# Kernel tuning notes

Hardware: AMD Instinct MI355X
Metric: run time of the kernel (lower is better)

Reference implementation:

```python
import jax, jax.numpy as jnp
import numpy as np

B, S, D_MODEL, H = 2, 2048, 1024, 16
HD = D_MODEL // H  # 64


def rotate_half(x):
    # pairs (x_even, x_odd) -> (-x_odd, x_even), interleaved back
    x1 = x[..., ::2]
    x2 = x[..., 1::2]
    return jnp.stack([-x2, x1], axis=-1).reshape(x.shape)


def rope_sin_cos(seq_len, head_dim):
    pos = jnp.arange(seq_len, dtype=jnp.float32)
    dim = jnp.arange(head_dim, dtype=jnp.float32)
    theta = 10000.0 ** (-2.0 * jnp.floor(dim / 2.0) / head_dim)
    angles = pos[:, None] * theta[None, :]  # [S, HD]
    return jnp.sin(angles), jnp.cos(angles)


def setup_inputs():
    key = jax.random.key(0)
    ks = jax.random.split(key, 6)
    w_scale = 1.0 / np.sqrt(D_MODEL)
    x = jax.random.normal(ks[0], (B, S, D_MODEL), jnp.float32)
    # causal mask: 1.0 where attention is disallowed (j > i)
    mask = (1.0 - jnp.tril(jnp.ones((S, S), jnp.float32)))[None, None, :, :]
    wq = jax.random.normal(ks[1], (D_MODEL, D_MODEL), jnp.float32) * w_scale
    wk = jax.random.normal(ks[2], (D_MODEL, D_MODEL), jnp.float32) * w_scale
    wv = jax.random.normal(ks[3], (D_MODEL, D_MODEL), jnp.float32) * w_scale
    wo = jax.random.normal(ks[4], (D_MODEL, D_MODEL), jnp.float32) * w_scale
    zeros = jnp.zeros((D_MODEL,), jnp.float32)
    return dict(x=x, mask=mask, wq=wq, bq=zeros, wk=wk, bk=zeros,
                wv=wv, bv=zeros, wo=wo, bo=zeros)


def reference(x, mask, wq, bq, wk, bk, wv, bv, wo, bo):
    b, s, _ = x.shape

    def split_heads(t):  # [B,S,D] -> [B,H,S,HD]
        return t.reshape(b, s, H, HD).transpose(0, 2, 1, 3)

    q = split_heads(x @ wq + bq)
    k = split_heads(x @ wk + bk)
    v = split_heads(x @ wv + bv)

    sin, cos = rope_sin_cos(s, HD)
    sin = sin[None, None, :, :]
    cos = cos[None, None, :, :]
    q = q * cos + rotate_half(q) * sin
    k = k * cos + rotate_half(k) * sin

    logits = jnp.einsum('bhqd,bhkd->bhqk', q, k) / jnp.sqrt(jnp.float32(HD))
    logits = logits + mask * (-1e9)
    attn = jax.nn.softmax(logits, axis=-1)
    out = jnp.einsum('bhqk,bhkd->bhqd', attn, v)  # [B,H,S,HD]
    out = out.transpose(0, 2, 1, 3).reshape(b, s, D_MODEL)
    return out @ wo + bo
```

## Files before the change

### kernel.cpp

```cpp
#include <hip/hip_runtime.h>
#include <hip/hip_bf16.h>


#define S_ 2048
#define DM 1024
#define HD 64

typedef __attribute__((ext_vector_type(8))) short short8;
typedef __attribute__((ext_vector_type(4))) float floatx4;

__device__ __forceinline__ unsigned short f2b(float x) {
  union { __hip_bfloat16 h; unsigned short u; } cv;
  cv.h = __float2bfloat16(x);
  return cv.u;
}

__device__ __forceinline__ void gload_lds16(const unsigned short* g, unsigned short* l) {
  typedef const __attribute__((address_space(1))) unsigned int* gp_t;
  typedef __attribute__((address_space(3))) unsigned int* lp_t;
  __builtin_amdgcn_global_load_lds((gp_t)(const void*)g, (lp_t)(void*)l, 16, 0, 0);
}

__global__ void prep_kernel(const float* __restrict__ x,
                            const float* __restrict__ w0, const float* __restrict__ w1,
                            const float* __restrict__ w2, const float* __restrict__ w3,
                            unsigned short* __restrict__ xc,
                            unsigned short* __restrict__ wt,
                            float2* __restrict__ rope) {
  const int bid = blockIdx.x;
  if (bid < 4096) {
    int i = (bid * 256 + threadIdx.x) * 4;
    float4 v = *(const float4*)(x + i);
    ushort4 o;
    o.x = f2b(v.x); o.y = f2b(v.y); o.z = f2b(v.z); o.w = f2b(v.w);
    *(ushort4*)(xc + i) = o;
  } else if (bid < 8192) {
    __shared__ float tile[32][33];
    const int rem = bid - 4096;
    const int z = rem >> 10;
    const int bx = (rem & 1023) & 31;
    const int by = (rem & 1023) >> 5;
    const float* W = (z == 0) ? w0 : (z == 1) ? w1 : (z == 2) ? w2 : w3;
    unsigned short* Wt = wt + (size_t)z * DM * DM;
    const int tx = threadIdx.x & 31;
    const int ty = threadIdx.x >> 5;
    const int k0 = bx * 32;
    const int c0 = by * 32;
#pragma unroll
    for (int i = 0; i < 4; ++i)
      tile[ty + i * 8][tx] = W[(size_t)(k0 + ty + i * 8) * DM + c0 + tx];
    __syncthreads();
#pragma unroll
    for (int i = 0; i < 4; ++i)
      Wt[(size_t)(c0 + ty + i * 8) * DM + k0 + tx] = f2b(tile[tx][ty + i * 8]);
  } else {
    int i = (bid - 8192) * 256 + threadIdx.x;
    int s = i >> 5, d2 = i & 31;
    float th = expf(-(float)d2 * (9.210340371976184f / 32.0f));
    float sn, cs;
    sincosf((float)s * th, &sn, &cs);
    rope[i] = make_float2(cs, sn);
  }
}

__global__ __launch_bounds__(256, 3) void gemm_qkv(
    const unsigned short* __restrict__ A, const unsigned short* __restrict__ Wt,
    const float* __restrict__ bq, const float* __restrict__ bk,
    const float* __restrict__ bv, const float2* __restrict__ rope,
    unsigned short* __restrict__ QKV) {
  __shared__ __attribute__((aligned(16))) unsigned short As[128 * 64];
  __shared__ __attribute__((aligned(16))) unsigned short Bs[128 * 64];
  const int r0 = blockIdx.x * 128;
  const int c0 = blockIdx.y * 128;
  const int t = threadIdx.x;
  const int lane = t & 63;
  const int wv = t >> 6;
  const int wr = (wv >> 1) * 64;
  const int wc = (wv & 1) * 64;
  const int lr = lane & 15;
  const int lg = lane >> 4;

  const int srow = wv * 32 + (lane >> 3);
  const int sseg = ((lane & 7) ^ (lane >> 3)) * 8;
  const unsigned short* Ag = A + (size_t)(r0 + srow) * DM + sseg;
  const unsigned short* Bg = Wt + (size_t)(c0 + srow) * DM + sseg;
  unsigned short* lA = &As[wv * 32 * 64];
  unsigned short* lB = &Bs[wv * 32 * 64];

  floatx4 acc[4][4] = {};
  const int fswz = (lr & 7) << 4;

  for (int k0 = 0; k0 < DM; k0 += 64) {
#pragma unroll
    for (int j = 0; j < 4; ++j) {
      gload_lds16(Ag + k0 + j * 8 * DM, lA + j * 8 * 64);
      gload_lds16(Bg + k0 + j * 8 * DM, lB + j * 8 * 64);
    }
    __syncthreads();
#pragma unroll
    for (int kk = 0; kk < 2; ++kk) {
      short8 af[4], bf[4];
#pragma unroll
      for (int m = 0; m < 4; ++m)
        af[m] = *(const short8*)((char*)As + (wr + m * 16 + lr) * 128 +
                                 ((kk * 64 + lg * 16) ^ fswz));
#pragma unroll
      for (int n = 0; n < 4; ++n)
        bf[n] = *(const short8*)((char*)Bs + (wc + n * 16 + lr) * 128 +
                                 ((kk * 64 + lg * 16) ^ fswz));
#pragma unroll
      for (int m = 0; m < 4; ++m)
#pragma unroll
        for (int n = 0; n < 4; ++n)
          acc[m][n] = __builtin_amdgcn_mfma_f32_16x16x32_bf16(af[m], bf[n], acc[m][n], 0, 0, 0);
    }
    __syncthreads();
  }

  const int mat = blockIdx.y >> 3;
  const float* bias = (mat == 0) ? bq : (mat == 1) ? bk : bv;
  const int rbase = r0 + wr + lg * 4;
  const int cbase = c0 + wc + lr;
#pragma unroll
  for (int n = 0; n < 4; ++n) {
    const int c = cbase + n * 16;
    const int cc = c & (DM - 1);
    const float bvv = bias[cc];
    const int d = c & 63;
    const int h = cc >> 6;
#pragma unroll
    for (int m = 0; m < 4; ++m) {
#pragma unroll
      for (int i = 0; i < 4; ++i) {
        const int r = rbase + m * 16 + i;
        const int s = r & (S_ - 1);
        const int b = r >> 11;
        float v = acc[m][n][i] + bvv;
        float pv = __shfl_xor(v, 1);
        if (mat < 2) {
          float2 cssn = rope[s * 32 + (d >> 1)];
          v = (d & 1) ? fmaf(v, cssn.x, pv * cssn.y) : fmaf(v, cssn.x, -pv * cssn.y);
          if (mat == 0) v *= 0.18033688011112042f;
        }
        QKV[((size_t)((mat << 5) | (b << 4) | h) * S_ + s) * HD + d] = f2b(v);
      }
    }
  }
}

__global__ __launch_bounds__(256, 3) void gemm_out(
    const unsigned short* __restrict__ A, const unsigned short* __restrict__ Wt,
    const float* __restrict__ bias, float* __restrict__ out) {
  __shared__ __attribute__((aligned(16))) unsigned short As[128 * 64];
  __shared__ __attribute__((aligned(16))) unsigned short Bs[128 * 64];
  const int r0 = blockIdx.x * 128;
  const int c0 = blockIdx.y * 128;
  const int t = threadIdx.x;
  const int lane = t & 63;
  const int wv = t >> 6;
  const int wr = (wv >> 1) * 64;
  const int wc = (wv & 1) * 64;
  const int lr = lane & 15;
  const int lg = lane >> 4;

  const int srow = wv * 32 + (lane >> 3);
  const int sseg = ((lane & 7) ^ (lane >> 3)) * 8;
  const unsigned short* Ag = A + (size_t)(r0 + srow) * DM + sseg;
  const unsigned short* Bg = Wt + (size_t)(c0 + srow) * DM + sseg;
  unsigned short* lA = &As[wv * 32 * 64];
  unsigned short* lB = &Bs[wv * 32 * 64];

  floatx4 acc[4][4] = {};
  const int fswz = (lr & 7) << 4;

  for (int k0 = 0; k0 < DM; k0 += 64) {
#pragma unroll
    for (int j = 0; j < 4; ++j) {
      gload_lds16(Ag + k0 + j * 8 * DM, lA + j * 8 * 64);
      gload_lds16(Bg + k0 + j * 8 * DM, lB + j * 8 * 64);
    }
    __syncthreads();
#pragma unroll
    for (int kk = 0; kk < 2; ++kk) {
      short8 af[4], bf[4];
#pragma unroll
      for (int m = 0; m < 4; ++m)
        af[m] = *(const short8*)((char*)As + (wr + m * 16 + lr) * 128 +
                                 ((kk * 64 + lg * 16) ^ fswz));
#pragma unroll
      for (int n = 0; n < 4; ++n)
        bf[n] = *(const short8*)((char*)Bs + (wc + n * 16 + lr) * 128 +
                                 ((kk * 64 + lg * 16) ^ fswz));
#pragma unroll
      for (int m = 0; m < 4; ++m)
#pragma unroll
        for (int n = 0; n < 4; ++n)
          acc[m][n] = __builtin_amdgcn_mfma_f32_16x16x32_bf16(af[m], bf[n], acc[m][n], 0, 0, 0);
    }
    __syncthreads();
  }

  const int rbase = r0 + wr + lg * 4;
  const int cbase = c0 + wc + lr;
#pragma unroll
  for (int n = 0; n < 4; ++n) {
    const int c = cbase + n * 16;
    const float bvv = bias[c];
#pragma unroll
    for (int m = 0; m < 4; ++m) {
#pragma unroll
      for (int i = 0; i < 4; ++i) {
        const int r = rbase + m * 16 + i;
        out[(size_t)r * DM + c] = acc[m][n][i] + bvv;
      }
    }
  }
}

#define ATTN_STEP(TT, BUF, KLA, KLB)                                           \
  do {                                                                         \
    {                  \
      char* Vb = (char*)Vs[BUF];                                               \
      const unsigned* ua = (const unsigned*)&va;                               \
      const unsigned* ub = (const unsigned*)&vb;                               \
      _Pragma("unroll") for (int j = 0; j < 8; ++j) {                          \
        unsigned pk = __builtin_amdgcn_perm(                                   \
            ub[j >> 1], ua[j >> 1], (j & 1) ? 0x07060302u : 0x05040100u);      \
        *(unsigned*)(Vb + (oct * 8 + j) * 128 + ((4 * kp) ^ (j << 4))) = pk;   \
      }                                                                        \
    }                                                                          \
    if ((TT) < qt) {                                \
      va = *(const short8*)(Vpref);                                            \
      vb = *(const short8*)(Vpref + 64);                                       \
      Vpref += 4096;                                                           \
    }                                                                          \
                        \
    asm volatile("s_waitcnt lgkmcnt(0)" ::: "memory");                         \
    __builtin_amdgcn_s_barrier();                                              \
                 \
    if ((TT) < qt) asm volatile("s_waitcnt vmcnt(2)" ::: "memory");            \
    else           asm volatile("s_waitcnt vmcnt(0)" ::: "memory");            \
    __builtin_amdgcn_sched_barrier(0);                                         \
    if ((TT) < qt) {                   \
      gload_lds16(Kpref, KLA);                                                 \
      gload_lds16(Kpref + 2048, KLB);                                          \
      Kpref += 4096;                                                           \
    }                                                                          \
                     \
    floatx4 s[4] = {};                                                         \
    __builtin_amdgcn_s_setprio(1);                                             \
    _Pragma("unroll") for (int kk = 0; kk < 2; ++kk) {                         \
      _Pragma("unroll") for (int n = 0; n < 4; ++n) {                          \
        int r = n * 16 + lr;                                                   \
        short8 kf = *(const short8*)((char*)Ks[BUF] + r * 128 +                \
                                     ((kk * 64 + lg * 16) ^ ((r & 7) << 4)));  \
        s[n] = __builtin_amdgcn_mfma_f32_16x16x32_bf16(kf, qf[kk], s[n], 0, 0, 0); \
      }                                                                        \
    }                                                                          \
    __builtin_amdgcn_s_setprio(0);                                             \
    if ((TT) == qt) {                                                          \
      _Pragma("unroll") for (int n = 0; n < 4; ++n)                            \
        _Pragma("unroll") for (int i = 0; i < 4; ++i)                          \
          if (n * 16 + lg * 4 + i > qin) s[n][i] = -1e30f;                     \
    }                                                                          \
                                \
    float ta = fmaxf(fmaxf(s[0][0], s[0][1]), s[0][2]);                        \
    float tb = fmaxf(fmaxf(s[0][3], s[1][0]), s[1][1]);                        \
    float tc = fmaxf(fmaxf(s[1][2], s[1][3]), s[2][0]);                        \
    float td = fmaxf(fmaxf(s[2][1], s[2][2]), s[2][3]);                        \
    float te = fmaxf(fmaxf(s[3][0], s[3][1]), s[3][2]);                        \
    float tm = fmaxf(fmaxf(ta, tb), tc);                                       \
    tm = fmaxf(fmaxf(tm, td), te);                                             \
    tm = fmaxf(tm, s[3][3]);                                                   \
    tm = fmaxf(tm, __shfl_xor(tm, 16));                                        \
    tm = fmaxf(tm, __shfl_xor(tm, 32));                                        \
    if (__any(tm > m + 8.f)) {                          \
      const float mn = fmaxf(m, tm);                                           \
      const float al = exp2f(m - mn);                                          \
      m = mn;                                                                  \
      lsum *= al;                                                              \
      _Pragma("unroll") for (int dd = 0; dd < 4; ++dd) o[dd] *= al;            \
    }                                                                          \
    float ps = 0.f;                                                            \
    _Pragma("unroll") for (int n = 0; n < 4; ++n) {                            \
      _Pragma("unroll") for (int i = 0; i < 4; ++i) {                          \
        float p = exp2f(s[n][i] - m);                                          \
        s[n][i] = p;                                                           \
        ps += p;                                                               \
      }                                                                        \
    }                                                                          \
    lsum += ps;                                                                \
                    \
    _Pragma("unroll") for (int n = 0; n < 4; ++n) {                            \
      _Pragma("unroll") for (int hh = 0; hh < 2; ++hh) {                       \
        unsigned pk = (unsigned)f2b(s[n][2 * hh]) |                            \
                      ((unsigned)f2b(s[n][2 * hh + 1]) << 16);                 \
        *(unsigned*)(Pw + lr * 128 +                                           \
                     (((n * 16 + lg * 4 + 2 * hh) * 2) ^ pswz)) = pk;          \
      }                                                                        \
    }                                                                          \
    short8 pb[2];                                                              \
    _Pragma("unroll") for (int kk = 0; kk < 2; ++kk)                           \
      pb[kk] = *(const short8*)(Pw + lr * 128 + ((kk * 64 + lg * 16) ^ pswz)); \
    __builtin_amdgcn_s_setprio(1);                                             \
    _Pragma("unroll") for (int kk = 0; kk < 2; ++kk)                           \
      _Pragma("unroll") for (int dd = 0; dd < 4; ++dd) {                       \
        int d = dd * 16 + lr;                                                  \
        short8 vbf = *(const short8*)((char*)Vs[BUF] + d * 128 +               \
                                      ((kk * 64 + lg * 16) ^ ((d & 7) << 4))); \
        o[dd] = __builtin_amdgcn_mfma_f32_16x16x32_bf16(vbf, pb[kk], o[dd], 0, 0, 0); \
      }                                                                        \
    __builtin_amdgcn_s_setprio(0);                                             \
  } while (0)

__global__ __launch_bounds__(256, 4) void attn_kernel(
    const unsigned short* __restrict__ Q, const unsigned short* __restrict__ K,
    const unsigned short* __restrict__ V, unsigned short* __restrict__ AttnC) {
  __shared__ __attribute__((aligned(16))) unsigned short Ks[2][64 * 64];
  __shared__ __attribute__((aligned(16))) unsigned short Vs[2][64 * 64];
  __shared__ __attribute__((aligned(16))) unsigned short Ps[4][16 * 64];

  const int bh = blockIdx.x;
  const int qt = 31 - (int)blockIdx.y;
  const int tid = threadIdx.x;
  const int w = tid >> 6;
  const int l = tid & 63;
  const int lg = l >> 4;
  const int lr = l & 15;
  const size_t base = (size_t)bh * S_ * HD;
  const int qin = w * 16 + lr;

  short8 qf[2];
  {
    const unsigned short* Qrow =
        Q + base + (size_t)(qt * 64 + w * 16 + lr) * HD + lg * 8;
    qf[0] = *(const short8*)(Qrow);
    qf[1] = *(const short8*)(Qrow + 32);
  }

  floatx4 o[4] = {};
  float m = -1e30f, lsum = 0.f;

  const int krow = tid >> 3;
  const int kseg = tid & 7;
  const unsigned short* Kpref = K + base + krow * 64 + ((kseg ^ (krow & 7)) * 8);
  unsigned short* const kld0a = &Ks[0][w * 512];
  unsigned short* const kld0b = &Ks[0][2048 + w * 512];
  unsigned short* const kld1a = &Ks[1][w * 512];
  unsigned short* const kld1b = &Ks[1][2048 + w * 512];

  const int oct = tid >> 5;
  const int kp = tid & 31;
  const unsigned short* Vpref = V + base + 2 * kp * 64 + oct * 8;

  short8 va = *(const short8*)(Vpref);
  short8 vb = *(const short8*)(Vpref + 64);
  Vpref += 4096;
  gload_lds16(Kpref, kld0a);
  gload_lds16(Kpref + 2048, kld0b);
  Kpref += 4096;

  char* const Pw = (char*)Ps[w];
  const int pswz = (lr & 7) << 4;

  int t = 0;
#pragma unroll 1
  for (; t + 1 <= qt; t += 2) {
    ATTN_STEP(t, 0, kld1a, kld1b);
    ATTN_STEP(t + 1, 1, kld0a, kld0b);
  }
  if (t <= qt) ATTN_STEP(t, 0, kld1a, kld1b);

  lsum += __shfl_xor(lsum, 16);
  lsum += __shfl_xor(lsum, 32);
  const float inv = 1.f / lsum;
  unsigned short* orow =
      AttnC + (size_t)((bh >> 4) * S_ + qt * 64 + w * 16 + lr) * DM + (bh & 15) * HD;
#pragma unroll
  for (int dd = 0; dd < 4; ++dd) {
    unsigned int w0 = (unsigned int)f2b(o[dd][0] * inv) |
                      ((unsigned int)f2b(o[dd][1] * inv) << 16);
    unsigned int w1 = (unsigned int)f2b(o[dd][2] * inv) |
                      ((unsigned int)f2b(o[dd][3] * inv) << 16);
    *(uint2*)(orow + dd * 16 + lg * 4) = make_uint2(w0, w1);
  }
}

extern "C" void kernel_launch(void* const* d_in, const int* in_sizes, int n_in,
                              void* d_out, int out_size, void* d_ws, size_t ws_size,
                              hipStream_t stream) {
  const float* x = (const float*)d_in[0];
  const float* wq = (const float*)d_in[2];
  const float* bq = (const float*)d_in[3];
  const float* wk = (const float*)d_in[4];
  const float* bk = (const float*)d_in[5];
  const float* wv = (const float*)d_in[6];
  const float* bv = (const float*)d_in[7];
  const float* wo = (const float*)d_in[8];
  const float* bo = (const float*)d_in[9];

  char* ws = (char*)d_ws;
  const size_t MB = 1024ull * 1024ull;
  unsigned short* Xc = (unsigned short*)(ws);
  unsigned short* Wt = (unsigned short*)(ws + 8 * MB);
  unsigned short* QKVb = (unsigned short*)(ws + 16 * MB);
  unsigned short* Ac = (unsigned short*)(ws + 40 * MB);
  float2* rope = (float2*)(ws + 48 * MB);

  prep_kernel<<<8448, 256, 0, stream>>>(x, wq, wk, wv, wo, Xc, Wt, rope);
  gemm_qkv<<<dim3(32, 24), 256, 0, stream>>>(Xc, Wt, bq, bk, bv, rope, QKVb);
  attn_kernel<<<dim3(32, 32), 256, 0, stream>>>(
      QKVb, QKVb + 32ull * S_ * HD, QKVb + 64ull * S_ * HD, Ac);
  gemm_out<<<dim3(32, 8), 256, 0, stream>>>(Ac, Wt + 3ull * DM * DM, bo, (float*)d_out);
}
```

Before: 114.3 us.

## Pair causal query tiles per block and switch attention to 32x32 MFMA

Each attention block now handles two query tiles, ya and 31-ya, with two waves per tile, so every block streams the same K/V range and the causal workload is balanced across the halved grid. QK and PV use 32x32x16 bf16 MFMAs, and the P operand is rearranged in registers with cross-lane shuffles instead of going through a per-wave LDS buffer. The diagonal tile skips the upper masked half for one sub-wave. Launch bounds drop to 2 blocks per CU, which raises register use and may reduce occupancy. Waves working on the shorter tile sit idle while the block continues loading tiles for the longer one.

New measurement: 126.5 us. 10.7% more time.

```diff
diff --git a/kernel.cpp b/kernel.cpp
--- a/kernel.cpp
+++ b/kernel.cpp
@@ -8,6 +8,7 @@
 
 typedef __attribute__((ext_vector_type(8))) short short8;
 typedef __attribute__((ext_vector_type(4))) float floatx4;
+typedef __attribute__((ext_vector_type(16))) float floatx16;
 
 __device__ __forceinline__ unsigned short f2b(float x) {
   union { __hip_bfloat16 h; unsigned short u; } cv;
@@ -217,6 +218,27 @@
   }
 }
 
+#define PVK(KSEG, PKS)                                                         \
+  do {                                                                         \
+    const int c4 = ((KSEG) & 1) * 4;                                           \
+    unsigned xv0 = hi ? (PKS)[c4 + 0] : (PKS)[c4 + 2];                         \
+    unsigned xv1 = hi ? (PKS)[c4 + 1] : (PKS)[c4 + 3];                         \
+    unsigned rv0 = (unsigned)__shfl_xor((int)xv0, 32);                         \
+    unsigned rv1 = (unsigned)__shfl_xor((int)xv1, 32);                         \
+    short8 bp;                                                                 \
+    unsigned* bpd = (unsigned*)&bp;                                            \
+    bpd[0] = hi ? rv0 : (PKS)[c4 + 0];                                         \
+    bpd[1] = hi ? rv1 : (PKS)[c4 + 1];                                         \
+    bpd[2] = hi ? (PKS)[c4 + 2] : rv0;                                         \
+    bpd[3] = hi ? (PKS)[c4 + 3] : rv1;                                         \
+    short8 vf0 = *(const short8*)(Vbb + q32 * 128 +                            \
+                                  (((KSEG)*32 + hi * 16) ^ kswz));             \
+    short8 vf1 = *(const short8*)(Vbb + (32 + q32) * 128 +                     \
+                                  (((KSEG)*32 + hi * 16) ^ kswz));             \
+    o0 = __builtin_amdgcn_mfma_f32_32x32x16_bf16(vf0, bp, o0, 0, 0, 0);        \
+    o1 = __builtin_amdgcn_mfma_f32_32x32x16_bf16(vf1, bp, o1, 0, 0, 0);        \
+  } while (0)
+
 #define ATTN_STEP(TT, BUF, KLA, KLB)                                           \
   do {                                                                         \
     {                  \
@@ -224,134 +246,150 @@
       const unsigned* ua = (const unsigned*)&va;                               \
       const unsigned* ub = (const unsigned*)&vb;                               \
       _Pragma("unroll") for (int j = 0; j < 8; ++j) {                          \
-        unsigned pk = __builtin_amdgcn_perm(                                   \
+        unsigned pkv = __builtin_amdgcn_perm(                                  \
             ub[j >> 1], ua[j >> 1], (j & 1) ? 0x07060302u : 0x05040100u);      \
-        *(unsigned*)(Vb + (oct * 8 + j) * 128 + ((4 * kp) ^ (j << 4))) = pk;   \
+        *(unsigned*)(Vb + (oct * 8 + j) * 128 + ((4 * kp) ^ (j << 4))) = pkv;  \
       }                                                                        \
     }                                                                          \
-    if ((TT) < qt) {                                \
+    if ((TT) < NTm1) {                              \
       va = *(const short8*)(Vpref);                                            \
       vb = *(const short8*)(Vpref + 64);                                       \
       Vpref += 4096;                                                           \
     }                                                                          \
-                        \
     asm volatile("s_waitcnt lgkmcnt(0)" ::: "memory");                         \
     __builtin_amdgcn_s_barrier();                                              \
-                 \
-    if ((TT) < qt) asm volatile("s_waitcnt vmcnt(2)" ::: "memory");            \
-    else           asm volatile("s_waitcnt vmcnt(0)" ::: "memory");            \
+    if ((TT) < NTm1) asm volatile("s_waitcnt vmcnt(2)" ::: "memory");          \
+    else             asm volatile("s_waitcnt vmcnt(0)" ::: "memory");          \
     __builtin_amdgcn_sched_barrier(0);                                         \
-    if ((TT) < qt) {                   \
+    if ((TT) < NTm1) {                 \
       gload_lds16(Kpref, KLA);                                                 \
       gload_lds16(Kpref + 2048, KLB);                                          \
       Kpref += 4096;                                                           \
     }                                                                          \
-                     \
-    floatx4 s[4] = {};                                                         \
-    __builtin_amdgcn_s_setprio(1);                                             \
-    _Pragma("unroll") for (int kk = 0; kk < 2; ++kk) {                         \
-      _Pragma("unroll") for (int n = 0; n < 4; ++n) {                          \
-        int r = n * 16 + lr;                                                   \
-        short8 kf = *(const short8*)((char*)Ks[BUF] + r * 128 +                \
-                                     ((kk * 64 + lg * 16) ^ ((r & 7) << 4)));  \
-        s[n] = __builtin_amdgcn_mfma_f32_16x16x32_bf16(kf, qf[kk], s[n], 0, 0, 0); \
-      }                                                                        \
+    if ((TT) <= myqs) {                                                        \
+      const bool diag = ((TT) == myqs);                                        \
+      const bool halfq = diag && (sub == 0);                                   \
+      const char* Kb = (const char*)Ks[BUF];                                   \
+      floatx16 s0 = {}, s1 = {};                                               \
+      __builtin_amdgcn_s_setprio(1);                                           \
+      _Pragma("unroll") for (int ds = 0; ds < 4; ++ds) {                       \
+        short8 kf = *(const short8*)(Kb + q32 * 128 +                          \
+                                     ((ds * 32 + hi * 16) ^ kswz));            \
+        s0 = __builtin_amdgcn_mfma_f32_32x32x16_bf16(kf, qf[ds], s0, 0, 0, 0); \
+      }                                                                        \
+      if (!halfq) {                                                            \
+        _Pragma("unroll") for (int ds = 0; ds < 4; ++ds) {                     \
+          short8 kf = *(const short8*)(Kb + (32 + q32) * 128 +                 \
+                                       ((ds * 32 + hi * 16) ^ kswz));          \
+          s1 = __builtin_amdgcn_mfma_f32_32x32x16_bf16(kf, qf[ds], s1, 0, 0, 0); \
+        }                                                                      \
+      }                                                                        \
+      __builtin_amdgcn_s_setprio(0);                                           \
+      if (diag) {        \
+        if (sub == 0) {                                                        \
+          _Pragma("unroll") for (int r = 0; r < 16; ++r) {                     \
+            int key32 = (r & 3) + 8 * (r >> 2) + 4 * hi;                       \
+            if (key32 > q32) s0[r] = -1e30f;                                   \
+          }                                                                    \
+        } else {                                                               \
+          _Pragma("unroll") for (int r = 0; r < 16; ++r) {                     \
+            int key32 = (r & 3) + 8 * (r >> 2) + 4 * hi;                       \
+            if (key32 > q32) s1[r] = -1e30f;                                   \
+          }                                                                    \
+        }                                                                      \
+      }                                                                        \
+              \
+      float tm = s0[0];                                                        \
+      _Pragma("unroll") for (int r = 1; r < 16; ++r) tm = fmaxf(tm, s0[r]);    \
+      if (!halfq) {                                                            \
+        _Pragma("unroll") for (int r = 0; r < 16; ++r) tm = fmaxf(tm, s1[r]);  \
+      }                                                                        \
+      tm = fmaxf(tm, __shfl_xor(tm, 32));                                      \
+      if (__any(tm > m + 8.f)) {                                               \
+        const float mn = fmaxf(m, tm);                                         \
+        const float al = exp2f(m - mn);                                        \
+        m = mn;                                                                \
+        lsum *= al;                                                            \
+        _Pragma("unroll") for (int r = 0; r < 16; ++r) {                       \
+          o0[r] *= al;                                                         \
+          o1[r] *= al;                                                         \
+        }                                                                      \
+      }                                                                        \
+      float ps = 0.f;                                                          \
+      _Pragma("unroll") for (int r = 0; r < 16; ++r) {                         \
+        float p = exp2f(s0[r] - m);                                            \
+        s0[r] = p;                                                             \
+        ps += p;                                                               \
+      }                                                                        \
+      if (!halfq) {                                                            \
+        _Pragma("unroll") for (int r = 0; r < 16; ++r) {                       \
+          float p = exp2f(s1[r] - m);                                          \
+          s1[r] = p;                                                           \
+          ps += p;                                                             \
+        }                                                                      \
+      }                                                                        \
+      lsum += ps;                                                              \
+                  \
+      unsigned pk0[8], pk1[8];                                                 \
+      _Pragma("unroll") for (int p = 0; p < 8; ++p)                            \
+        pk0[p] = (unsigned)f2b(s0[2 * p]) | ((unsigned)f2b(s0[2 * p + 1]) << 16); \
+      if (!halfq) {                                                            \
+        _Pragma("unroll") for (int p = 0; p < 8; ++p)                          \
+          pk1[p] = (unsigned)f2b(s1[2 * p]) | ((unsigned)f2b(s1[2 * p + 1]) << 16); \
+      }                                                                        \
+      const char* Vbb = (const char*)Vs[BUF];                                  \
+      __builtin_amdgcn_s_setprio(1);                                           \
+      PVK(0, pk0);                                                             \
+      PVK(1, pk0);                                                             \
+      if (!halfq) {                                                            \
+        PVK(2, pk1);                                                           \
+        PVK(3, pk1);                                                           \
+      }                                                                        \
+      __builtin_amdgcn_s_setprio(0);                                           \
     }                                                                          \
-    __builtin_amdgcn_s_setprio(0);                                             \
-    if ((TT) == qt) {                                                          \
-      _Pragma("unroll") for (int n = 0; n < 4; ++n)                            \
-        _Pragma("unroll") for (int i = 0; i < 4; ++i)                          \
-          if (n * 16 + lg * 4 + i > qin) s[n][i] = -1e30f;                     \
-    }                                                                          \
-                                \
-    float ta = fmaxf(fmaxf(s[0][0], s[0][1]), s[0][2]);                        \
-    float tb = fmaxf(fmaxf(s[0][3], s[1][0]), s[1][1]);                        \
-    float tc = fmaxf(fmaxf(s[1][2], s[1][3]), s[2][0]);                        \
-    float td = fmaxf(fmaxf(s[2][1], s[2][2]), s[2][3]);                        \
-    float te = fmaxf(fmaxf(s[3][0], s[3][1]), s[3][2]);                        \
-    float tm = fmaxf(fmaxf(ta, tb), tc);                                       \
-    tm = fmaxf(fmaxf(tm, td), te);                                             \
-    tm = fmaxf(tm, s[3][3]);                                                   \
-    tm = fmaxf(tm, __shfl_xor(tm, 16));                                        \
-    tm = fmaxf(tm, __shfl_xor(tm, 32));                                        \
-    if (__any(tm > m + 8.f)) {                          \
-      const float mn = fmaxf(m, tm);                                           \
-      const float al = exp2f(m - mn);                                          \
-      m = mn;                                                                  \
-      lsum *= al;                                                              \
-      _Pragma("unroll") for (int dd = 0; dd < 4; ++dd) o[dd] *= al;            \
-    }                                                                          \
-    float ps = 0.f;                                                            \
-    _Pragma("unroll") for (int n = 0; n < 4; ++n) {                            \
-      _Pragma("unroll") for (int i = 0; i < 4; ++i) {                          \
-        float p = exp2f(s[n][i] - m);                                          \
-        s[n][i] = p;                                                           \
-        ps += p;                                                               \
-      }                                                                        \
-    }                                                                          \
-    lsum += ps;                                                                \
-                    \
-    _Pragma("unroll") for (int n = 0; n < 4; ++n) {                            \
-      _Pragma("unroll") for (int hh = 0; hh < 2; ++hh) {                       \
-        unsigned pk = (unsigned)f2b(s[n][2 * hh]) |                            \
-                      ((unsigned)f2b(s[n][2 * hh + 1]) << 16);                 \
-        *(unsigned*)(Pw + lr * 128 +                                           \
-                     (((n * 16 + lg * 4 + 2 * hh) * 2) ^ pswz)) = pk;          \
-      }                                                                        \
-    }                                                                          \
-    short8 pb[2];                                                              \
-    _Pragma("unroll") for (int kk = 0; kk < 2; ++kk)                           \
-      pb[kk] = *(const short8*)(Pw + lr * 128 + ((kk * 64 + lg * 16) ^ pswz)); \
-    __builtin_amdgcn_s_setprio(1);                                             \
-    _Pragma("unroll") for (int kk = 0; kk < 2; ++kk)                           \
-      _Pragma("unroll") for (int dd = 0; dd < 4; ++dd) {                       \
-        int d = dd * 16 + lr;                                                  \
-        short8 vbf = *(const short8*)((char*)Vs[BUF] + d * 128 +               \
-                                      ((kk * 64 + lg * 16) ^ ((d & 7) << 4))); \
-        o[dd] = __builtin_amdgcn_mfma_f32_16x16x32_bf16(vbf, pb[kk], o[dd], 0, 0, 0); \
-      }                                                                        \
-    __builtin_amdgcn_s_setprio(0);                                             \
   } while (0)
 
-__global__ __launch_bounds__(256, 4) void attn_kernel(
+__global__ __launch_bounds__(256, 2) void attn_kernel(
     const unsigned short* __restrict__ Q, const unsigned short* __restrict__ K,
     const unsigned short* __restrict__ V, unsigned short* __restrict__ AttnC) {
   __shared__ __attribute__((aligned(16))) unsigned short Ks[2][64 * 64];
   __shared__ __attribute__((aligned(16))) unsigned short Vs[2][64 * 64];
-  __shared__ __attribute__((aligned(16))) unsigned short Ps[4][16 * 64];
 
   const int bh = blockIdx.x;
-  const int qt = 31 - (int)blockIdx.y;
+  const int ya = (int)blockIdx.y;
+  const int yb = 31 - ya;
   const int tid = threadIdx.x;
   const int w = tid >> 6;
-  const int l = tid & 63;
-  const int lg = l >> 4;
-  const int lr = l & 15;
+  const int lane = tid & 63;
+  const int hi = lane >> 5;
+  const int q32 = lane & 31;
+  const int kswz = (lane & 7) << 4;
+  const int sub = w & 1;
+  const int myqs = (w < 2) ? ya : yb;
+  const int NTm1 = yb;
   const size_t base = (size_t)bh * S_ * HD;
-  const int qin = w * 16 + lr;
-
-  short8 qf[2];
+
+  short8 qf[4];
   {
     const unsigned short* Qrow =
-        Q + base + (size_t)(qt * 64 + w * 16 + lr) * HD + lg * 8;
-    qf[0] = *(const short8*)(Qrow);
-    qf[1] = *(const short8*)(Qrow + 32);
-  }
-
-  floatx4 o[4] = {};
+        Q + base + (size_t)(myqs * 64 + sub * 32 + q32) * HD + hi * 8;
+#pragma unroll
+    for (int ds = 0; ds < 4; ++ds) qf[ds] = *(const short8*)(Qrow + ds * 16);
+  }
+
+  floatx16 o0 = {}, o1 = {};
   float m = -1e30f, lsum = 0.f;
 
   const int krow = tid >> 3;
-  const int kseg = tid & 7;
-  const unsigned short* Kpref = K + base + krow * 64 + ((kseg ^ (krow & 7)) * 8);
+  const int kseg8 = tid & 7;
+  const int oct = tid >> 5;
+  const int kp = tid & 31;
+  const unsigned short* Kpref = K + base + krow * 64 + ((kseg8 ^ (krow & 7)) * 8);
+  const unsigned short* Vpref = V + base + 2 * kp * 64 + oct * 8;
   unsigned short* const kld0a = &Ks[0][w * 512];
   unsigned short* const kld0b = &Ks[0][2048 + w * 512];
   unsigned short* const kld1a = &Ks[1][w * 512];
   unsigned short* const kld1b = &Ks[1][2048 + w * 512];
-
-  const int oct = tid >> 5;
-  const int kp = tid & 31;
-  const unsigned short* Vpref = V + base + 2 * kp * 64 + oct * 8;
 
   short8 va = *(const short8*)(Vpref);
   short8 vb = *(const short8*)(Vpref + 64);
@@ -360,29 +398,37 @@
   gload_lds16(Kpref + 2048, kld0b);
   Kpref += 4096;
 
-  char* const Pw = (char*)Ps[w];
-  const int pswz = (lr & 7) << 4;
-
   int t = 0;
 #pragma unroll 1
-  for (; t + 1 <= qt; t += 2) {
+  for (; t + 1 <= NTm1; t += 2) {
     ATTN_STEP(t, 0, kld1a, kld1b);
     ATTN_STEP(t + 1, 1, kld0a, kld0b);
   }
-  if (t <= qt) ATTN_STEP(t, 0, kld1a, kld1b);
-
-  lsum += __shfl_xor(lsum, 16);
+  if (t <= NTm1) ATTN_STEP(t, 0, kld1a, kld1b);
+
   lsum += __shfl_xor(lsum, 32);
   const float inv = 1.f / lsum;
+  const int qglob = myqs * 64 + sub * 32 + q32;
   unsigned short* orow =
-      AttnC + (size_t)((bh >> 4) * S_ + qt * 64 + w * 16 + lr) * DM + (bh & 15) * HD;
-#pragma unroll
-  for (int dd = 0; dd < 4; ++dd) {
-    unsigned int w0 = (unsigned int)f2b(o[dd][0] * inv) |
-                      ((unsigned int)f2b(o[dd][1] * inv) << 16);
-    unsigned int w1 = (unsigned int)f2b(o[dd][2] * inv) |
-                      ((unsigned int)f2b(o[dd][3] * inv) << 16);
-    *(uint2*)(orow + dd * 16 + lg * 4) = make_uint2(w0, w1);
+      AttnC + (size_t)((bh >> 4) * S_ + qglob) * DM + (bh & 15) * HD;
+#pragma unroll
+  for (int g = 0; g < 4; ++g) {
+    {
+      const int d0 = 8 * g + 4 * hi;
+      unsigned w0 = (unsigned)f2b(o0[4 * g + 0] * inv) |
+                    ((unsigned)f2b(o0[4 * g + 1] * inv) << 16);
+      unsigned w1 = (unsigned)f2b(o0[4 * g + 2] * inv) |
+                    ((unsigned)f2b(o0[4 * g + 3] * inv) << 16);
+      *(uint2*)(orow + d0) = make_uint2(w0, w1);
+    }
+    {
+      const int d0 = 32 + 8 * g + 4 * hi;
+      unsigned w0 = (unsigned)f2b(o1[4 * g + 0] * inv) |
+                    ((unsigned)f2b(o1[4 * g + 1] * inv) << 16);
+      unsigned w1 = (unsigned)f2b(o1[4 * g + 2] * inv) |
+                    ((unsigned)f2b(o1[4 * g + 3] * inv) << 16);
+      *(uint2*)(orow + d0) = make_uint2(w0, w1);
+    }
   }
 }
 
@@ -409,7 +455,7 @@
 
   prep_kernel<<<8448, 256, 0, stream>>>(x, wq, wk, wv, wo, Xc, Wt, rope);
   gemm_qkv<<<dim3(32, 24), 256, 0, stream>>>(Xc, Wt, bq, bk, bv, rope, QKVb);
-  attn_kernel<<<dim3(32, 32), 256, 0, stream>>>(
+  attn_kernel<<<dim3(32, 16), 256, 0, stream>>>(
       QKVb, QKVb + 32ull * S_ * HD, QKVb + 64ull * S_ * HD, Ac);
   gemm_out<<<dim3(32, 8), 256, 0, stream>>>(Ac, Wt + 3ull * DM * DM, bo, (float*)d_out);
 }
```

## Enlarge attention query tile to 128 rows with two row-groups per wave

Applied to the files above, without the earlier changes.

The attention kernel now processes 128 query rows per block instead of 64, with each wave handling two 16-row groups that share every K/V fragment loaded from LDS. This halves the K/V global and LDS traffic per query row and doubles the MFMA work per fragment load. Waves whose diagonal tile comes earlier skip compute on later key tiles. In exchange, register pressure roughly doubles (launch bounds drop from 4 to 2 blocks per CU), there are half as many blocks, and causal load imbalance inside a block grows.

After: 130.4 us. 14.1% more time.

```diff
diff --git a/kernel.cpp b/kernel.cpp
--- a/kernel.cpp
+++ b/kernel.cpp
@@ -224,134 +224,154 @@
       const unsigned* ua = (const unsigned*)&va;                               \
       const unsigned* ub = (const unsigned*)&vb;                               \
       _Pragma("unroll") for (int j = 0; j < 8; ++j) {                          \
-        unsigned pk = __builtin_amdgcn_perm(                                   \
+        unsigned pkv = __builtin_amdgcn_perm(                                  \
             ub[j >> 1], ua[j >> 1], (j & 1) ? 0x07060302u : 0x05040100u);      \
-        *(unsigned*)(Vb + (oct * 8 + j) * 128 + ((4 * kp) ^ (j << 4))) = pk;   \
+        *(unsigned*)(Vb + (oct * 8 + j) * 128 + ((4 * kp) ^ (j << 4))) = pkv;  \
       }                                                                        \
     }                                                                          \
-    if ((TT) < qt) {                                \
+    if ((TT) < NTm1) {                              \
       va = *(const short8*)(Vpref);                                            \
       vb = *(const short8*)(Vpref + 64);                                       \
       Vpref += 4096;                                                           \
     }                                                                          \
-                        \
     asm volatile("s_waitcnt lgkmcnt(0)" ::: "memory");                         \
     __builtin_amdgcn_s_barrier();                                              \
-                 \
-    if ((TT) < qt) asm volatile("s_waitcnt vmcnt(2)" ::: "memory");            \
-    else           asm volatile("s_waitcnt vmcnt(0)" ::: "memory");            \
+    if ((TT) < NTm1) asm volatile("s_waitcnt vmcnt(2)" ::: "memory");          \
+    else             asm volatile("s_waitcnt vmcnt(0)" ::: "memory");          \
     __builtin_amdgcn_sched_barrier(0);                                         \
-    if ((TT) < qt) {                   \
+    if ((TT) < NTm1) {                 \
       gload_lds16(Kpref, KLA);                                                 \
       gload_lds16(Kpref + 2048, KLB);                                          \
       Kpref += 4096;                                                           \
     }                                                                          \
-                     \
-    floatx4 s[4] = {};                                                         \
-    __builtin_amdgcn_s_setprio(1);                                             \
-    _Pragma("unroll") for (int kk = 0; kk < 2; ++kk) {                         \
+    if ((TT) <= dtw) {                                                         \
+                            \
+      floatx4 slo[4] = {}, shi[4] = {};                                        \
+      __builtin_amdgcn_s_setprio(1);                                           \
+      _Pragma("unroll") for (int kk = 0; kk < 2; ++kk) {                       \
+        _Pragma("unroll") for (int n = 0; n < 4; ++n) {                        \
+          int r = n * 16 + lr;                                                 \
+          short8 kf = *(const short8*)((char*)Ks[BUF] + r * 128 +              \
+                                       ((kk * 64 + lg * 16) ^ ((r & 7) << 4)));\
+          slo[n] = __builtin_amdgcn_mfma_f32_16x16x32_bf16(kf, qflo[kk], slo[n], 0, 0, 0); \
+          shi[n] = __builtin_amdgcn_mfma_f32_16x16x32_bf16(kf, qfhi[kk], shi[n], 0, 0, 0); \
+        }                                                                      \
+      }                                                                        \
+      __builtin_amdgcn_s_setprio(0);                                           \
+      if ((TT) == dtw) {                                      \
+        _Pragma("unroll") for (int n = 0; n < 4; ++n)                          \
+          _Pragma("unroll") for (int i = 0; i < 4; ++i) {                      \
+            int ki = n * 16 + lg * 4 + i;                                      \
+            if (ki > qinlo) slo[n][i] = -1e30f;                                \
+            if (ki > qinlo + 16) shi[n][i] = -1e30f;                           \
+          }                                                                    \
+      }                                                                        \
+                                       \
+      float tlo = fmaxf(fmaxf(slo[0][0], slo[0][1]), fmaxf(slo[0][2], slo[0][3])); \
+      float thi = fmaxf(fmaxf(shi[0][0], shi[0][1]), fmaxf(shi[0][2], shi[0][3])); \
+      _Pragma("unroll") for (int n = 1; n < 4; ++n) {                          \
+        tlo = fmaxf(tlo, fmaxf(fmaxf(slo[n][0], slo[n][1]),                    \
+                               fmaxf(slo[n][2], slo[n][3])));                  \
+        thi = fmaxf(thi, fmaxf(fmaxf(shi[n][0], shi[n][1]),                    \
+                               fmaxf(shi[n][2], shi[n][3])));                  \
+      }                                                                        \
+      tlo = fmaxf(tlo, __shfl_xor(tlo, 16));                                   \
+      tlo = fmaxf(tlo, __shfl_xor(tlo, 32));                                   \
+      thi = fmaxf(thi, __shfl_xor(thi, 16));                                   \
+      thi = fmaxf(thi, __shfl_xor(thi, 32));                                   \
+      if (__any((tlo > mlo + 8.f) || (thi > mhi + 8.f))) {                     \
+        const float nlo = fmaxf(mlo, tlo), nhi = fmaxf(mhi, thi);              \
+        const float alo = exp2f(mlo - nlo), ahi = exp2f(mhi - nhi);            \
+        mlo = nlo; mhi = nhi;                                                  \
+        llo *= alo; lhi *= ahi;                                                \
+        _Pragma("unroll") for (int dd = 0; dd < 4; ++dd) {                     \
+          olo[dd] *= alo;                                                      \
+          ohi[dd] *= ahi;                                                      \
+        }                                                                      \
+      }                                                                        \
+      float pslo = 0.f, pshi = 0.f;                                            \
       _Pragma("unroll") for (int n = 0; n < 4; ++n) {                          \
-        int r = n * 16 + lr;                                                   \
-        short8 kf = *(const short8*)((char*)Ks[BUF] + r * 128 +                \
-                                     ((kk * 64 + lg * 16) ^ ((r & 7) << 4)));  \
-        s[n] = __builtin_amdgcn_mfma_f32_16x16x32_bf16(kf, qf[kk], s[n], 0, 0, 0); \
-      }                                                                        \
+        _Pragma("unroll") for (int i = 0; i < 4; ++i) {                        \
+          float plo = exp2f(slo[n][i] - mlo);                                  \
+          float phi = exp2f(shi[n][i] - mhi);                                  \
+          slo[n][i] = plo; shi[n][i] = phi;                                    \
+          pslo += plo; pshi += phi;                                            \
+        }                                                                      \
+      }                                                                        \
+      llo += pslo; lhi += pshi;                                                \
+       \
+      _Pragma("unroll") for (int n = 0; n < 4; ++n) {                          \
+        _Pragma("unroll") for (int hh = 0; hh < 2; ++hh) {                     \
+          int cb = ((n * 16 + lg * 4 + 2 * hh) * 2) ^ pswz;                    \
+          unsigned plo = (unsigned)f2b(slo[n][2 * hh]) |                       \
+                         ((unsigned)f2b(slo[n][2 * hh + 1]) << 16);            \
+          unsigned phi = (unsigned)f2b(shi[n][2 * hh]) |                       \
+                         ((unsigned)f2b(shi[n][2 * hh + 1]) << 16);            \
+          *(unsigned*)(Pw + lr * 128 + cb) = plo;                              \
+          *(unsigned*)(Pw + (lr + 16) * 128 + cb) = phi;                       \
+        }                                                                      \
+      }                                                                        \
+      short8 pblo[2], pbhi[2];                                                 \
+      _Pragma("unroll") for (int kk = 0; kk < 2; ++kk) {                       \
+        pblo[kk] = *(const short8*)(Pw + lr * 128 + ((kk * 64 + lg * 16) ^ pswz)); \
+        pbhi[kk] = *(const short8*)(Pw + (lr + 16) * 128 + ((kk * 64 + lg * 16) ^ pswz)); \
+      }                                                                        \
+                             \
+      __builtin_amdgcn_s_setprio(1);                                           \
+      _Pragma("unroll") for (int kk = 0; kk < 2; ++kk)                         \
+        _Pragma("unroll") for (int dd = 0; dd < 4; ++dd) {                     \
+          int d = dd * 16 + lr;                                                \
+          short8 vbf = *(const short8*)((char*)Vs[BUF] + d * 128 +             \
+                                        ((kk * 64 + lg * 16) ^ ((d & 7) << 4))); \
+          olo[dd] = __builtin_amdgcn_mfma_f32_16x16x32_bf16(vbf, pblo[kk], olo[dd], 0, 0, 0); \
+          ohi[dd] = __builtin_amdgcn_mfma_f32_16x16x32_bf16(vbf, pbhi[kk], ohi[dd], 0, 0, 0); \
+        }                                                                      \
+      __builtin_amdgcn_s_setprio(0);                                           \
     }                                                                          \
-    __builtin_amdgcn_s_setprio(0);                                             \
-    if ((TT) == qt) {                                                          \
-      _Pragma("unroll") for (int n = 0; n < 4; ++n)                            \
-        _Pragma("unroll") for (int i = 0; i < 4; ++i)                          \
-          if (n * 16 + lg * 4 + i > qin) s[n][i] = -1e30f;                     \
-    }                                                                          \
-                                \
-    float ta = fmaxf(fmaxf(s[0][0], s[0][1]), s[0][2]);                        \
-    float tb = fmaxf(fmaxf(s[0][3], s[1][0]), s[1][1]);                        \
-    float tc = fmaxf(fmaxf(s[1][2], s[1][3]), s[2][0]);                        \
-    float td = fmaxf(fmaxf(s[2][1], s[2][2]), s[2][3]);                        \
-    float te = fmaxf(fmaxf(s[3][0], s[3][1]), s[3][2]);                        \
-    float tm = fmaxf(fmaxf(ta, tb), tc);                                       \
-    tm = fmaxf(fmaxf(tm, td), te);                                             \
-    tm = fmaxf(tm, s[3][3]);                                                   \
-    tm = fmaxf(tm, __shfl_xor(tm, 16));                                        \
-    tm = fmaxf(tm, __shfl_xor(tm, 32));                                        \
-    if (__any(tm > m + 8.f)) {                          \
-      const float mn = fmaxf(m, tm);                                           \
-      const float al = exp2f(m - mn);                                          \
-      m = mn;                                                                  \
-      lsum *= al;                                                              \
-      _Pragma("unroll") for (int dd = 0; dd < 4; ++dd) o[dd] *= al;            \
-    }                                                                          \
-    float ps = 0.f;                                                            \
-    _Pragma("unroll") for (int n = 0; n < 4; ++n) {                            \
-      _Pragma("unroll") for (int i = 0; i < 4; ++i) {                          \
-        float p = exp2f(s[n][i] - m);                                          \
-        s[n][i] = p;                                                           \
-        ps += p;                                                               \
-      }                                                                        \
-    }                                                                          \
-    lsum += ps;                                                                \
-                    \
-    _Pragma("unroll") for (int n = 0; n < 4; ++n) {                            \
-      _Pragma("unroll") for (int hh = 0; hh < 2; ++hh) {                       \
-        unsigned pk = (unsigned)f2b(s[n][2 * hh]) |                            \
-                      ((unsigned)f2b(s[n][2 * hh + 1]) << 16);                 \
-        *(unsigned*)(Pw + lr * 128 +                                           \
-                     (((n * 16 + lg * 4 + 2 * hh) * 2) ^ pswz)) = pk;          \
-      }                                                                        \
-    }                                                                          \
-    short8 pb[2];                                                              \
-    _Pragma("unroll") for (int kk = 0; kk < 2; ++kk)                           \
-      pb[kk] = *(const short8*)(Pw + lr * 128 + ((kk * 64 + lg * 16) ^ pswz)); \
-    __builtin_amdgcn_s_setprio(1);                                             \
-    _Pragma("unroll") for (int kk = 0; kk < 2; ++kk)                           \
-      _Pragma("unroll") for (int dd = 0; dd < 4; ++dd) {                       \
-        int d = dd * 16 + lr;                                                  \
-        short8 vbf = *(const short8*)((char*)Vs[BUF] + d * 128 +               \
-                                      ((kk * 64 + lg * 16) ^ ((d & 7) << 4))); \
-        o[dd] = __builtin_amdgcn_mfma_f32_16x16x32_bf16(vbf, pb[kk], o[dd], 0, 0, 0); \
-      }                                                                        \
-    __builtin_amdgcn_s_setprio(0);                                             \
   } while (0)
 
-__global__ __launch_bounds__(256, 4) void attn_kernel(
+__global__ __launch_bounds__(256, 2) void attn_kernel(
     const unsigned short* __restrict__ Q, const unsigned short* __restrict__ K,
     const unsigned short* __restrict__ V, unsigned short* __restrict__ AttnC) {
   __shared__ __attribute__((aligned(16))) unsigned short Ks[2][64 * 64];
   __shared__ __attribute__((aligned(16))) unsigned short Vs[2][64 * 64];
-  __shared__ __attribute__((aligned(16))) unsigned short Ps[4][16 * 64];
+  __shared__ __attribute__((aligned(16))) unsigned short Ps[4][32 * 64];
 
   const int bh = blockIdx.x;
-  const int qt = 31 - (int)blockIdx.y;
+  const int qt = 15 - (int)blockIdx.y;
   const int tid = threadIdx.x;
   const int w = tid >> 6;
   const int l = tid & 63;
   const int lg = l >> 4;
   const int lr = l & 15;
   const size_t base = (size_t)bh * S_ * HD;
-  const int qin = w * 16 + lr;
-
-  short8 qf[2];
+  const int NTm1 = 2 * qt + 1;
+  const int dtw = 2 * qt + (w >> 1);
+  const int qinlo = (w & 1) * 32 + lr;
+
+  short8 qflo[2], qfhi[2];
   {
-    const unsigned short* Qrow =
-        Q + base + (size_t)(qt * 64 + w * 16 + lr) * HD + lg * 8;
-    qf[0] = *(const short8*)(Qrow);
-    qf[1] = *(const short8*)(Qrow + 32);
-  }
-
-  floatx4 o[4] = {};
-  float m = -1e30f, lsum = 0.f;
+    const unsigned short* Qlo =
+        Q + base + (size_t)(qt * 128 + w * 32 + lr) * HD + lg * 8;
+    qflo[0] = *(const short8*)(Qlo);
+    qflo[1] = *(const short8*)(Qlo + 32);
+    qfhi[0] = *(const short8*)(Qlo + 16 * HD);
+    qfhi[1] = *(const short8*)(Qlo + 16 * HD + 32);
+  }
+
+  floatx4 olo[4] = {}, ohi[4] = {};
+  float mlo = -1e30f, mhi = -1e30f, llo = 0.f, lhi = 0.f;
 
   const int krow = tid >> 3;
-  const int kseg = tid & 7;
-  const unsigned short* Kpref = K + base + krow * 64 + ((kseg ^ (krow & 7)) * 8);
+  const int kseg8 = tid & 7;
+  const int oct = tid >> 5;
+  const int kp = tid & 31;
+  const unsigned short* Kpref = K + base + krow * 64 + ((kseg8 ^ (krow & 7)) * 8);
+  const unsigned short* Vpref = V + base + 2 * kp * 64 + oct * 8;
   unsigned short* const kld0a = &Ks[0][w * 512];
   unsigned short* const kld0b = &Ks[0][2048 + w * 512];
   unsigned short* const kld1a = &Ks[1][w * 512];
   unsigned short* const kld1b = &Ks[1][2048 + w * 512];
-
-  const int oct = tid >> 5;
-  const int kp = tid & 31;
-  const unsigned short* Vpref = V + base + 2 * kp * 64 + oct * 8;
 
   short8 va = *(const short8*)(Vpref);
   short8 vb = *(const short8*)(Vpref + 64);
@@ -363,26 +383,32 @@
   char* const Pw = (char*)Ps[w];
   const int pswz = (lr & 7) << 4;
 
-  int t = 0;
 #pragma unroll 1
-  for (; t + 1 <= qt; t += 2) {
+  for (int t = 0; t <= NTm1; t += 2) {
     ATTN_STEP(t, 0, kld1a, kld1b);
     ATTN_STEP(t + 1, 1, kld0a, kld0b);
   }
-  if (t <= qt) ATTN_STEP(t, 0, kld1a, kld1b);
-
-  lsum += __shfl_xor(lsum, 16);
-  lsum += __shfl_xor(lsum, 32);
-  const float inv = 1.f / lsum;
+
+  llo += __shfl_xor(llo, 16);
+  llo += __shfl_xor(llo, 32);
+  lhi += __shfl_xor(lhi, 16);
+  lhi += __shfl_xor(lhi, 32);
+  const float ilo = 1.f / llo;
+  const float ihi = 1.f / lhi;
   unsigned short* orow =
-      AttnC + (size_t)((bh >> 4) * S_ + qt * 64 + w * 16 + lr) * DM + (bh & 15) * HD;
+      AttnC + (size_t)((bh >> 4) * S_ + qt * 128 + w * 32 + lr) * DM + (bh & 15) * HD;
 #pragma unroll
   for (int dd = 0; dd < 4; ++dd) {
-    unsigned int w0 = (unsigned int)f2b(o[dd][0] * inv) |
-                      ((unsigned int)f2b(o[dd][1] * inv) << 16);
-    unsigned int w1 = (unsigned int)f2b(o[dd][2] * inv) |
-                      ((unsigned int)f2b(o[dd][3] * inv) << 16);
-    *(uint2*)(orow + dd * 16 + lg * 4) = make_uint2(w0, w1);
+    unsigned a0 = (unsigned)f2b(olo[dd][0] * ilo) |
+                  ((unsigned)f2b(olo[dd][1] * ilo) << 16);
+    unsigned a1 = (unsigned)f2b(olo[dd][2] * ilo) |
+                  ((unsigned)f2b(olo[dd][3] * ilo) << 16);
+    *(uint2*)(orow + dd * 16 + lg * 4) = make_uint2(a0, a1);
+    unsigned b0 = (unsigned)f2b(ohi[dd][0] * ihi) |
+                  ((unsigned)f2b(ohi[dd][1] * ihi) << 16);
+    unsigned b1 = (unsigned)f2b(ohi[dd][2] * ihi) |
+                  ((unsigned)f2b(ohi[dd][3] * ihi) << 16);
+    *(uint2*)(orow + 16 * DM + dd * 16 + lg * 4) = make_uint2(b0, b1);
   }
 }
 
@@ -409,7 +435,7 @@
 
   prep_kernel<<<8448, 256, 0, stream>>>(x, wq, wk, wv, wo, Xc, Wt, rope);
   gemm_qkv<<<dim3(32, 24), 256, 0, stream>>>(Xc, Wt, bq, bk, bv, rope, QKVb);
-  attn_kernel<<<dim3(32, 32), 256, 0, stream>>>(
+  attn_kernel<<<dim3(32, 16), 256, 0, stream>>>(
       QKVb, QKVb + 32ull * S_ * HD, QKVb + 64ull * S_ * HD, Ac);
   gemm_out<<<dim3(32, 8), 256, 0, stream>>>(Ac, Wt + 3ull * DM * DM, bo, (float*)d_out);
 }
```
